# Kernel tuning notes

Hardware: AMD Instinct MI355X
Metric: run time of the kernel (lower is better)

## Reference

```python
import jax, jax.numpy as jnp
import numpy as np

N = 262144   # tokens
L = 128      # ldims (per-direction LSTM feature size)
H = 128      # hidden_units
H2 = 128     # hidden2_units
R = 64       # number of relation labels


def setup_inputs() -> dict:
    key = jax.random.key(0)
    ks = jax.random.split(key, 12)
    glorot = lambda k, shape: jax.random.uniform(
        k, shape, jnp.float32, -1.0, 1.0) * np.sqrt(6.0 / (shape[0] + shape[1]))
    return {
        "fwd": jax.random.normal(ks[0], (N, L), jnp.float32),
        "bwd": jax.random.normal(ks[1], (N, L), jnp.float32),
        "gold_heads": jax.random.randint(ks[2], (N - 1,), 0, N),
        "gold_rels": jax.random.randint(ks[3], (N - 1,), 0, R),
        "WFOH": glorot(ks[4], (2 * L, H)),
        "WFOM": glorot(ks[5], (2 * L, H)),
        "rhidBias": glorot(ks[6], (1, H)),
        "rcatBias": glorot(ks[7], (1, 2 * H)),
        "rhid2Layer": glorot(ks[8], (2 * H, H2)),
        "rhid2Bias": glorot(ks[9], (1, H2)),
        "routLayer": glorot(ks[10], (H2, R)),
        "routBias": glorot(ks[11], (1, R)),
    }


def reference(fwd, bwd, gold_heads, gold_rels, WFOH, WFOM, rhidBias,
              rcatBias, rhid2Layer, rhid2Bias, routLayer, routBias):
    E = gold_heads.shape[0]
    mods = jnp.arange(E) + 1                       # modifiers are tokens 1..N-1
    # per-edge concat(head fwd-state, modifier bwd-state): (E, 2L)
    cat = jnp.concatenate([fwd[gold_heads], bwd[mods]], axis=-1)
    headfov = cat @ WFOH                           # (E, H)
    modfov = cat @ WFOM                            # (E, H)
    # hidden2_units > 0 branch of __evaluateLabel
    h = jnp.tanh(jnp.concatenate([headfov, modfov], axis=-1) + rcatBias)  # (E, 2H)
    h2 = jnp.tanh(h @ rhid2Layer + rhid2Bias)      # (E, H2)
    scores = h2 @ routLayer + routBias             # (E, R)
    # hinge: best wrong label vs gold label, loss only if margin violated
    gold_s = jnp.take_along_axis(scores, gold_rels[:, None], axis=1)[:, 0]
    masked = jnp.where(jnp.arange(R)[None, :] == gold_rels[:, None], -jnp.inf, scores)
    wrong_idx = jnp.argmax(masked, axis=1)
    wrong_s = jnp.take_along_axis(scores, wrong_idx[:, None], axis=1)[:, 0]
    lerrs = jnp.where(gold_s < wrong_s + 1.0, wrong_s - gold_s, 0.0)  # (E,)
    return lerrs
```

## Files before the change

kernel.cpp:

```cpp
#include <hip/hip_runtime.h>
#include <hip/hip_bf16.h>

typedef __bf16 bf16x8 __attribute__((ext_vector_type(8)));
typedef float  f32x4  __attribute__((ext_vector_type(4)));

#define MFMA16 __builtin_amdgcn_mfma_f32_16x16x32_bf16

__device__ __forceinline__ float fast_tanh(float x) {
    float e = __builtin_amdgcn_exp2f(x * 2.8853900817779268f);
    return 1.0f - 2.0f * __builtin_amdgcn_rcpf(e + 1.0f);
}

__device__ __forceinline__ int kinv(int ke) {
    return (ke & ~31) | ((ke & 1) << 4) | ((ke >> 1) & 15);
}

__device__ __forceinline__ bf16x8 cvt2(const float4 a, const float4 b) {
    bf16x8 t;
    t[0] = (__bf16)a.x; t[1] = (__bf16)a.y; t[2] = (__bf16)a.z; t[3] = (__bf16)a.w;
    t[4] = (__bf16)b.x; t[5] = (__bf16)b.y; t[6] = (__bf16)b.z; t[7] = (__bf16)b.w;
    return t;
}

__global__ __launch_bounds__(256) void preconv_kernel(
    const float* __restrict__ WFOH, const float* __restrict__ WFOM,
    const float* __restrict__ rhid2Layer, const float* __restrict__ routLayer,
    char* __restrict__ ws)
{
    const int f = blockIdx.x * 256 + threadIdx.x;
    bf16x8 v;
    char* dst;
    if (f < 8192) {
        const int lane = f & 63, t = f >> 6;
        const int nbl = t & 1, kk = (t >> 1) & 7, w = t >> 4;
        const int g = lane >> 4, c = lane & 15;
        const int nb = 32 * w + 16 * nbl;
        const float* Wsrc = (nb < 128) ? WFOH : WFOM;
        const int col = (nb + c) & 127;
        #pragma unroll
        for (int j = 0; j < 8; ++j) v[j] = (__bf16)Wsrc[(32 * kk + 8 * g + j) * 128 + col];
        dst = ws + (size_t)f * 16;
    } else if (f < 12288) {
        const int f2 = f - 8192;
        const int lane = f2 & 63, t = f2 >> 6;
        const int nbl = t & 1, kk = (t >> 1) & 7, q4 = t >> 4;
        const int g = lane >> 4, c = lane & 15;
        const int n2 = 32 * q4 + 16 * nbl + c;
        #pragma unroll
        for (int j = 0; j < 8; ++j) v[j] = (__bf16)rhid2Layer[kinv(32 * kk + 8 * g + j) * 128 + n2];
        dst = ws + 131072 + (size_t)f2 * 16;
    } else if (f < 13312) {
        const int f3 = f - 12288;
        const int lane = f3 & 63, t = f3 >> 6;
        const int kk = t & 3, q4 = t >> 2;
        const int g = lane >> 4, c = lane & 15;
        const int n3 = 16 * q4 + c;
        #pragma unroll
        for (int j = 0; j < 8; ++j) v[j] = (__bf16)routLayer[kinv(32 * kk + 8 * g + j) * 64 + n3];
        dst = ws + 196608 + (size_t)f3 * 16;
    } else {
        return;
    }
    *(bf16x8*)dst = v;
}

template<bool PRE>
__device__ __forceinline__ bf16x8 wfrag1(const char* ws, const float* WFOH, const float* WFOM,
                                         int w, int kk, int nbl, int lane) {
    if constexpr (PRE) {
        return *(const bf16x8*)(ws + (size_t)w * 16384 + kk * 2048 + nbl * 1024 + lane * 16);
    } else {
        const int g = lane >> 4, c = lane & 15;
        const int nb = 32 * w + 16 * nbl;
        const float* Wsrc = (nb < 128) ? WFOH : WFOM;
        const int col = (nb + c) & 127;
        bf16x8 v;
        #pragma unroll
        for (int j = 0; j < 8; ++j) v[j] = (__bf16)Wsrc[(32 * kk + 8 * g + j) * 128 + col];
        return v;
    }
}
template<bool PRE>
__device__ __forceinline__ bf16x8 wfrag2(const char* ws, const float* rhid2Layer,
                                         int q4, int kk, int nbl, int lane) {
    if constexpr (PRE) {
        return *(const bf16x8*)(ws + 131072 + (size_t)q4 * 16384 + kk * 2048 + nbl * 1024 + lane * 16);
    } else {
        const int g = lane >> 4, c = lane & 15;
        const int n2 = 32 * q4 + 16 * nbl + c;
        bf16x8 v;
        #pragma unroll
        for (int j = 0; j < 8; ++j) v[j] = (__bf16)rhid2Layer[kinv(32 * kk + 8 * g + j) * 128 + n2];
        return v;
    }
}
template<bool PRE>
__device__ __forceinline__ bf16x8 wfrag3(const char* ws, const float* routLayer,
                                         int q4, int kk, int lane) {
    if constexpr (PRE) {
        return *(const bf16x8*)(ws + 196608 + (size_t)q4 * 4096 + kk * 1024 + lane * 16);
    } else {
        const int g = lane >> 4, c = lane & 15;
        const int n3 = 16 * q4 + c;
        bf16x8 v;
        #pragma unroll
        for (int j = 0; j < 8; ++j) v[j] = (__bf16)routLayer[kinv(32 * kk + 8 * g + j) * 64 + n3];
        return v;
    }
}

template<bool PRE>
__global__ __launch_bounds__(512, 2) void rel_kernel(
    const float* __restrict__ fwd, const float* __restrict__ bwd,
    const int* __restrict__ gold_heads, const int* __restrict__ gold_rels,
    const float* __restrict__ WFOH, const float* __restrict__ WFOM,
    const float* __restrict__ rcatBias, const float* __restrict__ rhid2Layer,
    const float* __restrict__ rhid2Bias, const float* __restrict__ routLayer,
    const float* __restrict__ routBias, const char* __restrict__ ws,
    int* __restrict__ fixcnt, int* __restrict__ fixlist, int fixcap,
    float* __restrict__ out, int E, int NT)
{
    __shared__ __align__(16) char smem[65536];

    char* const sh_cat = smem;
    char* const sh_h   = smem + 32768;
    char* const sh_h2  = smem;
    char* const sh_sc  = smem + 32768;

    const int tid   = threadIdx.x;
    const int w     = tid >> 6;
    const int lane  = tid & 63;
    const int row16 = lane & 15;
    const int g     = lane >> 4;
    const int xm    = (row16 & 7) << 4;
    const int mw    = w >> 2;
    const int nw    = w & 3;

    const int r_s = tid >> 3;
    const int q_s = tid & 7;
    const int xr  = (r_s & 7) << 4;

    const float rcb0 = rcatBias[32 * w + row16];
    const float rcb1 = rcatBias[32 * w + 16 + row16];
    const float r2b  = rhid2Bias[16 * w + row16];
    const float rob  = routBias[16 * nw + row16];

    bf16x8 pfb[4];
    {
        const int e = blockIdx.x * 64 + r_s;
        int nh = 0;
        if (q_s < 4 && e < E) nh = gold_heads[e];
        if (e < E) {
            const float* src = (q_s < 4) ? (fwd + (size_t)nh * 128 + 32 * q_s)
                                         : (bwd + (size_t)(e + 1) * 128 + 32 * (q_s - 4));
            const float4* p4 = (const float4*)src;
            #pragma unroll
            for (int i = 0; i < 4; ++i) pfb[i] = cvt2(p4[2 * i], p4[2 * i + 1]);
        } else {
            #pragma unroll
            for (int i = 0; i < 4; ++i) pfb[i] = cvt2(make_float4(0.f,0.f,0.f,0.f), make_float4(0.f,0.f,0.f,0.f));
        }
    }

    for (int tile = blockIdx.x; tile < NT; tile += gridDim.x) {
        const int e0 = tile * 64;
        const int tnext = tile + gridDim.x;
        const bool hn = tnext < NT;

        #pragma unroll
        for (int i = 0; i < 4; ++i)
            *(bf16x8*)(sh_cat + r_s * 512 + ((64 * q_s + 16 * i) ^ xr)) = pfb[i];

        int nh = 0;
        bool gv = false;
        if (hn) {
            const int en = tnext * 64 + r_s;
            gv = en < E;
            if (q_s < 4 && gv) nh = gold_heads[en];
        }
        __syncthreads();

        f32x4 acc1[4][2];
        #pragma unroll
        for (int i = 0; i < 4; ++i) {
            acc1[i][0] = (f32x4){0.f, 0.f, 0.f, 0.f};
            acc1[i][1] = (f32x4){0.f, 0.f, 0.f, 0.f};
        }
        {
            bf16x8 b0 = wfrag1<PRE>(ws, WFOH, WFOM, w, 0, 0, lane);
            bf16x8 b1 = wfrag1<PRE>(ws, WFOH, WFOM, w, 0, 1, lane);
            #pragma unroll 1
            for (int kk = 0; kk < 8; ++kk) {
                const bf16x8 nb0 = wfrag1<PRE>(ws, WFOH, WFOM, w, (kk + 1) & 7, 0, lane);
                const bf16x8 nb1 = wfrag1<PRE>(ws, WFOH, WFOM, w, (kk + 1) & 7, 1, lane);
                const int ko = (64 * kk + 16 * g) ^ xm;
                #pragma unroll
                for (int mb = 0; mb < 4; ++mb) {
                    const bf16x8 a = *(const bf16x8*)(sh_cat + (16 * mb + row16) * 512 + ko);
                    acc1[mb][0] = MFMA16(a, b0, acc1[mb][0], 0, 0, 0);
                    acc1[mb][1] = MFMA16(a, b1, acc1[mb][1], 0, 0, 0);
                }
                b0 = nb0; b1 = nb1;
            }
        }
        #pragma unroll
        for (int mb = 0; mb < 4; ++mb) {
            #pragma unroll
            for (int r = 0; r < 4; ++r) {
                const int row = 16 * mb + 4 * g + r;
                __bf16 p0 = (__bf16)fast_tanh(acc1[mb][0][r] + rcb0);
                __bf16 p1 = (__bf16)fast_tanh(acc1[mb][1][r] + rcb1);
                unsigned short u0 = __builtin_bit_cast(unsigned short, p0);
                unsigned short u1 = __builtin_bit_cast(unsigned short, p1);
                *(unsigned*)(sh_h + row * 512 + ((64 * w + 4 * row16) ^ ((row & 7) << 4)))
                    = (unsigned)u0 | ((unsigned)u1 << 16);
            }
        }
        __syncthreads();

        const float* gsrc = nullptr;
        if (hn) {
            const int en = tnext * 64 + r_s;
            gsrc = (q_s < 4) ? (fwd + (size_t)nh * 128 + 32 * q_s)
                             : (bwd + (size_t)(en + 1) * 128 + 32 * (q_s - 4));
        }
        float4 pfA[4];
        if (hn && gv) {
            const float4* p4 = (const float4*)gsrc;
            #pragma unroll
            for (int i = 0; i < 4; ++i) pfA[i] = p4[i];
        } else {
            #pragma unroll
            for (int i = 0; i < 4; ++i) pfA[i] = make_float4(0.f, 0.f, 0.f, 0.f);
        }

        f32x4 acc2[4];
        #pragma unroll
        for (int i = 0; i < 4; ++i) acc2[i] = (f32x4){0.f, 0.f, 0.f, 0.f};
        {
            bf16x8 b2 = wfrag2<PRE>(ws, rhid2Layer, w >> 1, 0, w & 1, lane);
            #pragma unroll 1
            for (int kk = 0; kk < 8; ++kk) {
                const bf16x8 nb2 = wfrag2<PRE>(ws, rhid2Layer, w >> 1, (kk + 1) & 7, w & 1, lane);
                const int ko = (64 * kk + 16 * g) ^ xm;
                #pragma unroll
                for (int mb = 0; mb < 4; ++mb) {
                    const bf16x8 a = *(const bf16x8*)(sh_h + (16 * mb + row16) * 512 + ko);
                    acc2[mb] = MFMA16(a, b2, acc2[mb], 0, 0, 0);
                }
                b2 = nb2;
            }
        }
        pfb[0] = cvt2(pfA[0], pfA[1]);
        pfb[1] = cvt2(pfA[2], pfA[3]);
        float4 pfB[4];
        if (hn && gv) {
            const float4* p4 = (const float4*)gsrc;
            #pragma unroll
            for (int i = 0; i < 4; ++i) pfB[i] = p4[4 + i];
        } else {
            #pragma unroll
            for (int i = 0; i < 4; ++i) pfB[i] = make_float4(0.f, 0.f, 0.f, 0.f);
        }
        #pragma unroll
        for (int mb = 0; mb < 4; ++mb) {
            #pragma unroll
            for (int r = 0; r < 4; ++r) {
                const int row = 16 * mb + 4 * g + r;
                __bf16 p = (__bf16)fast_tanh(acc2[mb][r] + r2b);
                *(unsigned short*)(sh_h2 + row * 256 +
                    ((64 * (w >> 1) + 4 * row16 + 2 * (w & 1)) ^ ((row & 7) << 4)))
                    = __builtin_bit_cast(unsigned short, p);
            }
        }
        __syncthreads();

        f32x4 acc3[2];
        acc3[0] = (f32x4){0.f, 0.f, 0.f, 0.f};
        acc3[1] = (f32x4){0.f, 0.f, 0.f, 0.f};
        #pragma unroll
        for (int kk = 0; kk < 4; ++kk) {
            const bf16x8 b = wfrag3<PRE>(ws, routLayer, nw, kk, lane);
            const int ko = (64 * kk + 16 * g) ^ xm;
            #pragma unroll
            for (int i = 0; i < 2; ++i) {
                const bf16x8 a = *(const bf16x8*)(sh_h2 + (32 * mw + 16 * i + row16) * 256 + ko);
                acc3[i] = MFMA16(a, b, acc3[i], 0, 0, 0);
            }
        }
        pfb[2] = cvt2(pfB[0], pfB[1]);
        pfb[3] = cvt2(pfB[2], pfB[3]);
        #pragma unroll
        for (int i = 0; i < 2; ++i) {
            #pragma unroll
            for (int r = 0; r < 4; ++r) {
                const int row = 32 * mw + 16 * i + 4 * g + r;
                const int col = 16 * nw + row16;
                *(float*)(sh_sc + row * 256 + ((4 * col) ^ ((row & 7) << 4))) = acc3[i][r] + rob;
            }
        }
        __syncthreads();

        {
            const int r = tid >> 3, q = tid & 7;
            const int e = e0 + r;
            const int gold = (e < E) ? gold_rels[e] : 0;
            const int xrh = (r & 7) << 4;
            const f32x4 s0 = *(const f32x4*)(sh_sc + r * 256 + ((32 * q) ^ xrh));
            const f32x4 s1 = *(const f32x4*)(sh_sc + r * 256 + ((32 * q + 16) ^ xrh));
            float gs = -3.0e38f, ws_ = -3.0e38f;
            #pragma unroll
            for (int cc = 0; cc < 4; ++cc) {
                const int lab0 = 8 * q + cc, lab1 = 8 * q + 4 + cc;
                if (lab0 == gold) gs = s0[cc]; else ws_ = fmaxf(ws_, s0[cc]);
                if (lab1 == gold) gs = s1[cc]; else ws_ = fmaxf(ws_, s1[cc]);
            }
            gs = fmaxf(gs, __shfl_xor(gs, 1)); ws_ = fmaxf(ws_, __shfl_xor(ws_, 1));
            gs = fmaxf(gs, __shfl_xor(gs, 2)); ws_ = fmaxf(ws_, __shfl_xor(ws_, 2));
            gs = fmaxf(gs, __shfl_xor(gs, 4)); ws_ = fmaxf(ws_, __shfl_xor(ws_, 4));
            if (q == 0 && e < E) {
                out[e] = (gs < ws_ + 1.0f) ? (ws_ - gs) : 0.0f;
                if (fabsf((gs - ws_) - 1.0f) < 0.125f && fixcap > 0) {
                    const int idx = atomicAdd(fixcnt, 1);
                    if (idx < fixcap) fixlist[idx] = e;
                }
            }
        }
    }
}

__global__ __launch_bounds__(256) void fixup_kernel(
    const float* __restrict__ fwd, const float* __restrict__ bwd,
    const int* __restrict__ gold_heads, const int* __restrict__ gold_rels,
    const float* __restrict__ WFOH, const float* __restrict__ WFOM,
    const float* __restrict__ rcatBias, const float* __restrict__ rhid2Layer,
    const float* __restrict__ rhid2Bias, const float* __restrict__ routLayer,
    const float* __restrict__ routBias,
    const int* __restrict__ fixcnt, const int* __restrict__ fixlist, int fixcap,
    float* __restrict__ out)
{
    __shared__ float fx_cat[256];
    __shared__ float fx_h[256];
    __shared__ float fx_h2[128];
    __shared__ float fx_p[256];
    int n = *fixcnt;
    if (n > fixcap) n = fixcap;
    const int tid = threadIdx.x;
    for (int i = blockIdx.x; i < n; i += gridDim.x) {
        const int e = fixlist[i];
        {
            const int head = gold_heads[e];
            fx_cat[tid] = (tid < 128) ? fwd[(size_t)head * 128 + tid]
                                      : bwd[(size_t)(e + 1) * 128 + (tid - 128)];
        }
        __syncthreads();
        {
            const float* base = (tid < 128) ? WFOH : WFOM;
            const int col = tid & 127;
            float s = 0.f;
            #pragma unroll 8
            for (int k = 0; k < 256; ++k) s += fx_cat[k] * base[k * 128 + col];
            fx_h[tid] = tanhf(s + rcatBias[tid]);
        }
        __syncthreads();
        {
            const int d = tid & 127, hh = tid >> 7;
            float s = 0.f;
            #pragma unroll 8
            for (int k = 128 * hh; k < 128 * hh + 128; ++k) s += fx_h[k] * rhid2Layer[k * 128 + d];
            fx_p[hh * 128 + d] = s;
        }
        __syncthreads();
        if (tid < 128) fx_h2[tid] = tanhf(fx_p[tid] + fx_p[128 + tid] + rhid2Bias[tid]);
        __syncthreads();
        {
            const int d = tid & 63, qq = tid >> 6;
            float s = 0.f;
            #pragma unroll 8
            for (int k = 32 * qq; k < 32 * qq + 32; ++k) s += fx_h2[k] * routLayer[k * 64 + d];
            fx_p[qq * 64 + d] = s;
        }
        __syncthreads();
        if (tid < 64) {
            const float v = fx_p[tid] + fx_p[64 + tid] + fx_p[128 + tid] + fx_p[192 + tid] + routBias[tid];
            const int gold = gold_rels[e];
            float gs = (tid == gold) ? v : -3.0e38f;
            float wv = (tid == gold) ? -3.0e38f : v;
            #pragma unroll
            for (int o = 1; o < 64; o <<= 1) {
                gs = fmaxf(gs, __shfl_xor(gs, o));
                wv = fmaxf(wv, __shfl_xor(wv, o));
            }
            if (tid == 0) out[e] = (gs < wv + 1.0f) ? (wv - gs) : 0.0f;
        }
        __syncthreads();
    }
}

extern "C" void kernel_launch(void* const* d_in, const int* in_sizes, int n_in,
                              void* d_out, int out_size, void* d_ws, size_t ws_size,
                              hipStream_t stream) {
    const float* fwd        = (const float*)d_in[0];
    const float* bwd        = (const float*)d_in[1];
    const int*   gold_heads = (const int*)d_in[2];
    const int*   gold_rels  = (const int*)d_in[3];
    const float* WFOH       = (const float*)d_in[4];
    const float* WFOM       = (const float*)d_in[5];
    const float* rcatBias   = (const float*)d_in[7];
    const float* rhid2      = (const float*)d_in[8];
    const float* rhid2Bias  = (const float*)d_in[9];
    const float* rout       = (const float*)d_in[10];
    const float* routBias   = (const float*)d_in[11];
    float* out = (float*)d_out;

    const int E = in_sizes[2];
    if (E <= 0) return;
    const int NT = (E + 63) / 64;
    const int grid = NT < 512 ? NT : 512;

    const size_t TAB = 212992;
    const int FIXCAP = 8192;
    const size_t FIX_BYTES = 4 + 4 * (size_t)FIXCAP;

    bool pre = ws_size >= TAB + FIX_BYTES;
    int* fixcnt = nullptr;
    int* fixlist = nullptr;
    int fixcap = 0;
    if (pre) {
        fixcnt = (int*)((char*)d_ws + TAB);
        fixlist = fixcnt + 1;
        fixcap = FIXCAP;
    } else if (ws_size >= FIX_BYTES) {
        fixcnt = (int*)d_ws;
        fixlist = fixcnt + 1;
        fixcap = FIXCAP;
    }
    if (fixcap) hipMemsetAsync(fixcnt, 0, 4, stream);

    if (pre) {
        hipLaunchKernelGGL(preconv_kernel, dim3(52), dim3(256), 0, stream,
                           WFOH, WFOM, rhid2, rout, (char*)d_ws);
        hipLaunchKernelGGL((rel_kernel<true>), dim3(grid), dim3(512), 0, stream,
                           fwd, bwd, gold_heads, gold_rels, WFOH, WFOM, rcatBias,
                           rhid2, rhid2Bias, rout, routBias, (const char*)d_ws,
                           fixcnt, fixlist, fixcap, out, E, NT);
    } else {
        hipLaunchKernelGGL((rel_kernel<false>), dim3(grid), dim3(512), 0, stream,
                           fwd, bwd, gold_heads, gold_rels, WFOH, WFOM, rcatBias,
                           rhid2, rhid2Bias, rout, routBias, (const char*)nullptr,
                           fixcnt, fixlist, fixcap, out, E, NT);
    }
    if (fixcap) {
        hipLaunchKernelGGL(fixup_kernel, dim3(120), dim3(256), 0, stream,
                           fwd, bwd, gold_heads, gold_rels, WFOH, WFOM, rcatBias,
                           rhid2, rhid2Bias, rout, routBias,
                           fixcnt, fixlist, fixcap, out);
    }
}
```

Measured before the change: 186.5 us.

## Restructure rel_kernel tail: register-resident scoring, earlier prefetch, fewer barriers

Layer 3 now runs in four waves, each computing all 64 labels for 16 rows. The hinge reduction happens in registers with lane shuffles, which removes the score round-trip through shared memory and one barrier. The whole next-tile gather (8 float4) is issued right after the first barrier so it overlaps the two big GEMMs, and gold_rels is loaded early. The weight-fragment loops are fully unrolled, with an asm-opaque zero offset to keep the loads in the loop. Shared memory grows to 80KB and register pressure rises, which may limit occupancy at 2 blocks/CU, and half the waves sit idle during layer 3.

```diff
diff --git a/kernel.cpp b/kernel.cpp
--- a/kernel.cpp
+++ b/kernel.cpp
@@ -96,12 +96,12 @@
 }
 template<bool PRE>
 __device__ __forceinline__ bf16x8 wfrag3(const char* ws, const float* routLayer,
-                                         int q4, int kk, int lane) {
+                                         int nb, int kk, int lane) {
     if constexpr (PRE) {
-        return *(const bf16x8*)(ws + 196608 + (size_t)q4 * 4096 + kk * 1024 + lane * 16);
+        return *(const bf16x8*)(ws + 196608 + (size_t)nb * 4096 + kk * 1024 + lane * 16);
     } else {
         const int g = lane >> 4, c = lane & 15;
-        const int n3 = 16 * q4 + c;
+        const int n3 = 16 * nb + c;
         bf16x8 v;
         #pragma unroll
         for (int j = 0; j < 8; ++j) v[j] = (__bf16)routLayer[kinv(32 * kk + 8 * g + j) * 64 + n3];
@@ -116,16 +116,14 @@
     const float* __restrict__ WFOH, const float* __restrict__ WFOM,
     const float* __restrict__ rcatBias, const float* __restrict__ rhid2Layer,
     const float* __restrict__ rhid2Bias, const float* __restrict__ routLayer,
-    const float* __restrict__ routBias, const char* __restrict__ ws,
+    const float* __restrict__ routBias, const char* __restrict__ wstab,
     int* __restrict__ fixcnt, int* __restrict__ fixlist, int fixcap,
     float* __restrict__ out, int E, int NT)
 {
-    __shared__ __align__(16) char smem[65536];
-
+    __shared__ __align__(16) char smem[81920];
     char* const sh_cat = smem;
     char* const sh_h   = smem + 32768;
-    char* const sh_h2  = smem;
-    char* const sh_sc  = smem + 32768;
+    char* const sh_h2  = smem + 65536;
 
     const int tid   = threadIdx.x;
     const int w     = tid >> 6;
@@ -133,8 +131,6 @@
     const int row16 = lane & 15;
     const int g     = lane >> 4;
     const int xm    = (row16 & 7) << 4;
-    const int mw    = w >> 2;
-    const int nw    = w & 3;
 
     const int r_s = tid >> 3;
     const int q_s = tid & 7;
@@ -143,15 +139,17 @@
     const float rcb0 = rcatBias[32 * w + row16];
     const float rcb1 = rcatBias[32 * w + 16 + row16];
     const float r2b  = rhid2Bias[16 * w + row16];
-    const float rob  = routBias[16 * nw + row16];
+    float rob[4];
+    #pragma unroll
+    for (int nb = 0; nb < 4; ++nb) rob[nb] = routBias[16 * nb + row16];
 
     bf16x8 pfb[4];
     {
         const int e = blockIdx.x * 64 + r_s;
-        int nh = 0;
-        if (q_s < 4 && e < E) nh = gold_heads[e];
+        int nh0 = 0;
+        if (q_s < 4 && e < E) nh0 = gold_heads[e];
         if (e < E) {
-            const float* src = (q_s < 4) ? (fwd + (size_t)nh * 128 + 32 * q_s)
+            const float* src = (q_s < 4) ? (fwd + (size_t)nh0 * 128 + 32 * q_s)
                                          : (bwd + (size_t)(e + 1) * 128 + 32 * (q_s - 4));
             const float4* p4 = (const float4*)src;
             #pragma unroll
@@ -167,18 +165,46 @@
         const int tnext = tile + gridDim.x;
         const bool hn = tnext < NT;
 
-        #pragma unroll
-        for (int i = 0; i < 4; ++i)
-            *(bf16x8*)(sh_cat + r_s * 512 + ((64 * q_s + 16 * i) ^ xr)) = pfb[i];
-
-        int nh = 0;
-        bool gv = false;
+        int zoff = 0;
+        asm volatile("" : "+v"(zoff));
+        const char*  wsL  = wstab + zoff;
+        const float* W1aL = WFOH + zoff;
+        const float* W1bL = WFOM + zoff;
+        const float* W2L  = rhid2Layer + zoff;
+        const float* W3L  = routLayer + zoff;
+
+        int nh = 0; bool gv = false;
         if (hn) {
             const int en = tnext * 64 + r_s;
             gv = en < E;
             if (q_s < 4 && gv) nh = gold_heads[en];
         }
-        __syncthreads();
+
+        #pragma unroll
+        for (int i = 0; i < 4; ++i)
+            *(bf16x8*)(sh_cat + r_s * 512 + ((64 * q_s + 16 * i) ^ xr)) = pfb[i];
+
+        int gr[4] = {0, 0, 0, 0};
+        if (w < 4) {
+            #pragma unroll
+            for (int i = 0; i < 4; ++i) {
+                const int e = e0 + 16 * w + 4 * g + i;
+                if (e < E) gr[i] = gold_rels[e];
+            }
+        }
+        __syncthreads();
+
+        float4 pfA[8];
+        if (hn && gv) {
+            const float4* p4 = (const float4*)((q_s < 4)
+                                 ? (fwd + (size_t)nh * 128 + 32 * q_s)
+                                 : (bwd + (size_t)(tnext * 64 + r_s + 1) * 128 + 32 * (q_s - 4)));
+            #pragma unroll
+            for (int i = 0; i < 8; ++i) pfA[i] = p4[i];
+        } else {
+            #pragma unroll
+            for (int i = 0; i < 8; ++i) pfA[i] = make_float4(0.f, 0.f, 0.f, 0.f);
+        }
 
         f32x4 acc1[4][2];
         #pragma unroll
@@ -186,21 +212,16 @@
             acc1[i][0] = (f32x4){0.f, 0.f, 0.f, 0.f};
             acc1[i][1] = (f32x4){0.f, 0.f, 0.f, 0.f};
         }
-        {
-            bf16x8 b0 = wfrag1<PRE>(ws, WFOH, WFOM, w, 0, 0, lane);
-            bf16x8 b1 = wfrag1<PRE>(ws, WFOH, WFOM, w, 0, 1, lane);
-            #pragma unroll 1
-            for (int kk = 0; kk < 8; ++kk) {
-                const bf16x8 nb0 = wfrag1<PRE>(ws, WFOH, WFOM, w, (kk + 1) & 7, 0, lane);
-                const bf16x8 nb1 = wfrag1<PRE>(ws, WFOH, WFOM, w, (kk + 1) & 7, 1, lane);
-                const int ko = (64 * kk + 16 * g) ^ xm;
-                #pragma unroll
-                for (int mb = 0; mb < 4; ++mb) {
-                    const bf16x8 a = *(const bf16x8*)(sh_cat + (16 * mb + row16) * 512 + ko);
-                    acc1[mb][0] = MFMA16(a, b0, acc1[mb][0], 0, 0, 0);
-                    acc1[mb][1] = MFMA16(a, b1, acc1[mb][1], 0, 0, 0);
-                }
-                b0 = nb0; b1 = nb1;
+        #pragma unroll
+        for (int kk = 0; kk < 8; ++kk) {
+            const bf16x8 b0 = wfrag1<PRE>(wsL, W1aL, W1bL, w, kk, 0, lane);
+            const bf16x8 b1 = wfrag1<PRE>(wsL, W1aL, W1bL, w, kk, 1, lane);
+            const int ko = (64 * kk + 16 * g) ^ xm;
+            #pragma unroll
+            for (int mb = 0; mb < 4; ++mb) {
+                const bf16x8 a = *(const bf16x8*)(sh_cat + (16 * mb + row16) * 512 + ko);
+                acc1[mb][0] = MFMA16(a, b0, acc1[mb][0], 0, 0, 0);
+                acc1[mb][1] = MFMA16(a, b1, acc1[mb][1], 0, 0, 0);
             }
         }
         #pragma unroll
@@ -208,121 +229,79 @@
             #pragma unroll
             for (int r = 0; r < 4; ++r) {
                 const int row = 16 * mb + 4 * g + r;
-                __bf16 p0 = (__bf16)fast_tanh(acc1[mb][0][r] + rcb0);
-                __bf16 p1 = (__bf16)fast_tanh(acc1[mb][1][r] + rcb1);
-                unsigned short u0 = __builtin_bit_cast(unsigned short, p0);
-                unsigned short u1 = __builtin_bit_cast(unsigned short, p1);
-                *(unsigned*)(sh_h + row * 512 + ((64 * w + 4 * row16) ^ ((row & 7) << 4)))
-                    = (unsigned)u0 | ((unsigned)u1 << 16);
-            }
-        }
-        __syncthreads();
-
-        const float* gsrc = nullptr;
-        if (hn) {
-            const int en = tnext * 64 + r_s;
-            gsrc = (q_s < 4) ? (fwd + (size_t)nh * 128 + 32 * q_s)
-                             : (bwd + (size_t)(en + 1) * 128 + 32 * (q_s - 4));
-        }
-        float4 pfA[4];
-        if (hn && gv) {
-            const float4* p4 = (const float4*)gsrc;
-            #pragma unroll
-            for (int i = 0; i < 4; ++i) pfA[i] = p4[i];
-        } else {
-            #pragma unroll
-            for (int i = 0; i < 4; ++i) pfA[i] = make_float4(0.f, 0.f, 0.f, 0.f);
-        }
+                const __bf16 p0 = (__bf16)fast_tanh(acc1[mb][0][r] + rcb0);
+                const __bf16 p1 = (__bf16)fast_tanh(acc1[mb][1][r] + rcb1);
+                const unsigned u = (unsigned)__builtin_bit_cast(unsigned short, p0)
+                                 | ((unsigned)__builtin_bit_cast(unsigned short, p1) << 16);
+                *(unsigned*)(sh_h + row * 512 + ((64 * w + 4 * row16) ^ ((row & 7) << 4))) = u;
+            }
+        }
+        __syncthreads();
 
         f32x4 acc2[4];
         #pragma unroll
         for (int i = 0; i < 4; ++i) acc2[i] = (f32x4){0.f, 0.f, 0.f, 0.f};
-        {
-            bf16x8 b2 = wfrag2<PRE>(ws, rhid2Layer, w >> 1, 0, w & 1, lane);
-            #pragma unroll 1
-            for (int kk = 0; kk < 8; ++kk) {
-                const bf16x8 nb2 = wfrag2<PRE>(ws, rhid2Layer, w >> 1, (kk + 1) & 7, w & 1, lane);
-                const int ko = (64 * kk + 16 * g) ^ xm;
-                #pragma unroll
-                for (int mb = 0; mb < 4; ++mb) {
-                    const bf16x8 a = *(const bf16x8*)(sh_h + (16 * mb + row16) * 512 + ko);
-                    acc2[mb] = MFMA16(a, b2, acc2[mb], 0, 0, 0);
-                }
-                b2 = nb2;
-            }
-        }
-        pfb[0] = cvt2(pfA[0], pfA[1]);
-        pfb[1] = cvt2(pfA[2], pfA[3]);
-        float4 pfB[4];
-        if (hn && gv) {
-            const float4* p4 = (const float4*)gsrc;
-            #pragma unroll
-            for (int i = 0; i < 4; ++i) pfB[i] = p4[4 + i];
-        } else {
-            #pragma unroll
-            for (int i = 0; i < 4; ++i) pfB[i] = make_float4(0.f, 0.f, 0.f, 0.f);
+        #pragma unroll
+        for (int kk = 0; kk < 8; ++kk) {
+            const bf16x8 b2 = wfrag2<PRE>(wsL, W2L, w >> 1, kk, w & 1, lane);
+            const int ko = (64 * kk + 16 * g) ^ xm;
+            #pragma unroll
+            for (int mb = 0; mb < 4; ++mb) {
+                const bf16x8 a = *(const bf16x8*)(sh_h + (16 * mb + row16) * 512 + ko);
+                acc2[mb] = MFMA16(a, b2, acc2[mb], 0, 0, 0);
+            }
         }
         #pragma unroll
         for (int mb = 0; mb < 4; ++mb) {
             #pragma unroll
             for (int r = 0; r < 4; ++r) {
                 const int row = 16 * mb + 4 * g + r;
-                __bf16 p = (__bf16)fast_tanh(acc2[mb][r] + r2b);
+                const __bf16 p = (__bf16)fast_tanh(acc2[mb][r] + r2b);
                 *(unsigned short*)(sh_h2 + row * 256 +
                     ((64 * (w >> 1) + 4 * row16 + 2 * (w & 1)) ^ ((row & 7) << 4)))
                     = __builtin_bit_cast(unsigned short, p);
             }
         }
-        __syncthreads();
-
-        f32x4 acc3[2];
-        acc3[0] = (f32x4){0.f, 0.f, 0.f, 0.f};
-        acc3[1] = (f32x4){0.f, 0.f, 0.f, 0.f};
-        #pragma unroll
-        for (int kk = 0; kk < 4; ++kk) {
-            const bf16x8 b = wfrag3<PRE>(ws, routLayer, nw, kk, lane);
-            const int ko = (64 * kk + 16 * g) ^ xm;
-            #pragma unroll
-            for (int i = 0; i < 2; ++i) {
-                const bf16x8 a = *(const bf16x8*)(sh_h2 + (32 * mw + 16 * i + row16) * 256 + ko);
-                acc3[i] = MFMA16(a, b, acc3[i], 0, 0, 0);
-            }
-        }
-        pfb[2] = cvt2(pfB[0], pfB[1]);
-        pfb[3] = cvt2(pfB[2], pfB[3]);
-        #pragma unroll
-        for (int i = 0; i < 2; ++i) {
-            #pragma unroll
-            for (int r = 0; r < 4; ++r) {
-                const int row = 32 * mw + 16 * i + 4 * g + r;
-                const int col = 16 * nw + row16;
-                *(float*)(sh_sc + row * 256 + ((4 * col) ^ ((row & 7) << 4))) = acc3[i][r] + rob;
-            }
-        }
-        __syncthreads();
-
-        {
-            const int r = tid >> 3, q = tid & 7;
-            const int e = e0 + r;
-            const int gold = (e < E) ? gold_rels[e] : 0;
-            const int xrh = (r & 7) << 4;
-            const f32x4 s0 = *(const f32x4*)(sh_sc + r * 256 + ((32 * q) ^ xrh));
-            const f32x4 s1 = *(const f32x4*)(sh_sc + r * 256 + ((32 * q + 16) ^ xrh));
-            float gs = -3.0e38f, ws_ = -3.0e38f;
-            #pragma unroll
-            for (int cc = 0; cc < 4; ++cc) {
-                const int lab0 = 8 * q + cc, lab1 = 8 * q + 4 + cc;
-                if (lab0 == gold) gs = s0[cc]; else ws_ = fmaxf(ws_, s0[cc]);
-                if (lab1 == gold) gs = s1[cc]; else ws_ = fmaxf(ws_, s1[cc]);
-            }
-            gs = fmaxf(gs, __shfl_xor(gs, 1)); ws_ = fmaxf(ws_, __shfl_xor(ws_, 1));
-            gs = fmaxf(gs, __shfl_xor(gs, 2)); ws_ = fmaxf(ws_, __shfl_xor(ws_, 2));
-            gs = fmaxf(gs, __shfl_xor(gs, 4)); ws_ = fmaxf(ws_, __shfl_xor(ws_, 4));
-            if (q == 0 && e < E) {
-                out[e] = (gs < ws_ + 1.0f) ? (ws_ - gs) : 0.0f;
-                if (fabsf((gs - ws_) - 1.0f) < 0.125f && fixcap > 0) {
-                    const int idx = atomicAdd(fixcnt, 1);
-                    if (idx < fixcap) fixlist[idx] = e;
+        #pragma unroll
+        for (int i = 0; i < 4; ++i) pfb[i] = cvt2(pfA[2 * i], pfA[2 * i + 1]);
+        __syncthreads();
+
+        if (w < 4) {
+            bf16x8 a3[4];
+            #pragma unroll
+            for (int kk = 0; kk < 4; ++kk)
+                a3[kk] = *(const bf16x8*)(sh_h2 + (16 * w + row16) * 256 + ((64 * kk + 16 * g) ^ xm));
+            f32x4 acc3[4];
+            #pragma unroll
+            for (int nb = 0; nb < 4; ++nb) {
+                acc3[nb] = (f32x4){0.f, 0.f, 0.f, 0.f};
+                #pragma unroll
+                for (int kk = 0; kk < 4; ++kk) {
+                    const bf16x8 b = wfrag3<PRE>(wsL, W3L, nb, kk, lane);
+                    acc3[nb] = MFMA16(a3[kk], b, acc3[nb], 0, 0, 0);
+                }
+            }
+            #pragma unroll
+            for (int i = 0; i < 4; ++i) {
+                const int gold = gr[i];
+                float gs = -3.0e38f, ws_ = -3.0e38f;
+                #pragma unroll
+                for (int nb = 0; nb < 4; ++nb) {
+                    const float v = acc3[nb][i] + rob[nb];
+                    const int lab = 16 * nb + row16;
+                    if (lab == gold) gs = v; else ws_ = fmaxf(ws_, v);
+                }
+                gs = fmaxf(gs, __shfl_xor(gs, 1)); ws_ = fmaxf(ws_, __shfl_xor(ws_, 1));
+                gs = fmaxf(gs, __shfl_xor(gs, 2)); ws_ = fmaxf(ws_, __shfl_xor(ws_, 2));
+                gs = fmaxf(gs, __shfl_xor(gs, 4)); ws_ = fmaxf(ws_, __shfl_xor(ws_, 4));
+                gs = fmaxf(gs, __shfl_xor(gs, 8)); ws_ = fmaxf(ws_, __shfl_xor(ws_, 8));
+                const int e = e0 + 16 * w + 4 * g + i;
+                if (row16 == 0 && e < E) {
+                    out[e] = (gs < ws_ + 1.0f) ? (ws_ - gs) : 0.0f;
+                    if (fabsf((gs - ws_) - 1.0f) < 0.125f && fixcap > 0) {
+                        const int idx = atomicAdd(fixcnt, 1);
+                        if (idx < fixcap) fixlist[idx] = e;
+                    }
                 }
             }
         }
@@ -422,7 +401,7 @@
     const int FIXCAP = 8192;
     const size_t FIX_BYTES = 4 + 4 * (size_t)FIXCAP;
 
-    bool pre = ws_size >= TAB + FIX_BYTES;
+    const bool pre = ws_size >= TAB + FIX_BYTES;
     int* fixcnt = nullptr;
     int* fixlist = nullptr;
     int fixcap = 0;
```

Result: no change. 185.4 us (-0.6%).
